# Performance work log

Hardware: AMD Instinct MI355X
Metric: run time of the kernel (lower is better)

## Reference

```python
import jax, jax.numpy as jnp
import numpy as np

B = 8
DIM = 256          # __init__ dim; input has 2*DIM channels
H = 32
W = 32
NUM_HEADS = 4
DH_QK = 64         # make_divisible(256*1.0, 8) // 4
DH_V = 64          # dim_out // num_heads
DQK = NUM_HEADS * DH_QK   # 256
DV = NUM_HEADS * DH_V     # 256
SCALE = DH_QK ** -0.5
HIDDEN = 4 * DIM          # mlp_ratio=4 applied to dim
DIM_OUT = DIM
EPS = 1e-5


def setup_inputs() -> dict:
    key = jax.random.key(0)
    ks = jax.random.split(key, 8)
    qkv_out = 2 * DQK + DV   # 768
    return {
        "x": jax.random.normal(ks[0], (B, 2 * DIM, H, W), jnp.float32),
        "qkv_f_w": jax.random.normal(ks[1], (qkv_out, DIM), jnp.float32) * DIM ** -0.5,
        "qkv_p_w": jax.random.normal(ks[2], (qkv_out, DIM), jnp.float32) * DIM ** -0.5,
        "height_rel": jax.random.normal(ks[3], (2 * H - 1, DH_QK), jnp.float32) * SCALE,
        "width_rel": jax.random.normal(ks[4], (2 * W - 1, DH_QK), jnp.float32) * SCALE,
        "ln_gamma": jnp.ones((2 * DV, H, W), jnp.float32),
        "ln_beta": jnp.zeros((2 * DV, H, W), jnp.float32),
        "fc1_w": jax.random.normal(ks[5], (HIDDEN, 2 * DV), jnp.float32) * (2 * DV) ** -0.5,
        "fc1_b": jnp.zeros((HIDDEN,), jnp.float32),
        "fc2_w": jax.random.normal(ks[6], (DIM_OUT, HIDDEN), jnp.float32) * HIDDEN ** -0.5,
        "fc2_b": jnp.zeros((DIM_OUT,), jnp.float32),
    }


def _rel_to_abs(x):
    # x: (b, L, 2L-1) -> (b, L, L) via the pad/reshape shift trick
    b, L, _ = x.shape
    x = jnp.pad(x, ((0, 0), (0, 0), (0, 1)))          # (b, L, 2L)
    xf = x.reshape(b, L * 2 * L)
    xf = jnp.pad(xf, ((0, 0), (0, L - 1)))
    return xf.reshape(b, L + 1, 2 * L - 1)[:, :L, L - 1:]


def _rel_logits_1d(q, rel_k, perm):
    # q: (b, h, w, d); rel_k: (2w-1, d) -> (b, h, w, h, w) after perm
    b, h, w, _ = q.shape
    x = jnp.einsum('bhwd,md->bhwm', q, rel_k).reshape(b * h, w, 2 * w - 1)
    x = _rel_to_abs(x).reshape(b, h, 1, w, w)
    x = jnp.broadcast_to(x, (b, h, h, w, w))
    return x.transpose(perm)


def _pos_embed(q, height_rel, width_rel):
    # q: (B*nh, HW, d) -> relative-position logits (B*nh, HW, HW)
    bh = q.shape[0]
    qs = q.reshape(bh, H, W, DH_QK)
    lw = _rel_logits_1d(qs, width_rel, (0, 1, 3, 2, 4))
    lh = _rel_logits_1d(qs.transpose(0, 2, 1, 3), height_rel, (0, 3, 1, 4, 2))
    return (lh + lw).reshape(bh, H * W, H * W)


def _get_qkv(x, w):
    # 1x1 conv as channel GEMM; x: (B, DIM, H, W)
    qkv = jnp.einsum('bchw,oc->bohw', x, w)
    q, k, v = jnp.split(qkv, [DQK, 2 * DQK], axis=1)
    q = q.reshape(B * NUM_HEADS, DH_QK, H * W).transpose(0, 2, 1)  # (Bh, HW, d)
    k = k.reshape(B * NUM_HEADS, DH_QK, H * W)                      # (Bh, d, HW)
    v = v.reshape(B * NUM_HEADS, DH_V, H * W).transpose(0, 2, 1)    # (Bh, HW, d)
    return q, k, v


def _apply_attn(q, k, v, height_rel, width_rel):
    logits = jnp.einsum('bnd,bdm->bnm', q, k) * SCALE + _pos_embed(q, height_rel, width_rel)
    attn = jax.nn.softmax(logits, axis=-1)
    out = jnp.einsum('bnm,bmd->bnd', attn, v)                       # (Bh, HW, dv)
    return out.transpose(0, 2, 1).reshape(B, DV, H, W)


def reference(x, qkv_f_w, qkv_p_w, height_rel, width_rel, ln_gamma, ln_beta,
              fc1_w, fc1_b, fc2_w, fc2_b):
    x1, x2 = x[:, :DIM], x[:, DIM:]
    qf, kf, vf = _get_qkv(x1, qkv_f_w)
    qp, kp, vp = _get_qkv(x2, qkv_p_w)
    out_f = _apply_attn(qf, kp, vp, height_rel, width_rel)
    out_p = _apply_attn(qp, kf, vf, height_rel, width_rel)
    xpf = jnp.concatenate([out_f, out_p], axis=1)                   # (B, 2*DV, H, W)
    # LayerNorm over normalized_shape = [2*DV, H, W]
    mean = xpf.mean(axis=(1, 2, 3), keepdims=True)
    var = jnp.var(xpf, axis=(1, 2, 3), keepdims=True)
    xpf = (xpf - mean) * jax.lax.rsqrt(var + EPS) * ln_gamma + ln_beta
    # conv-MLP (1x1 convs), exact GELU as torch default
    h = jnp.einsum('bchw,oc->bohw', xpf, fc1_w) + fc1_b[None, :, None, None]
    h = jax.nn.gelu(h, approximate=False)
    out = jnp.einsum('bchw,oc->bohw', h, fc2_w) + fc2_b[None, :, None, None]
    return out  # stride=1 -> pool is identity
```

## Files before the change

kernel.cpp:

```cpp
#include <hip/hip_runtime.h>

#define SCALE 0.125f

typedef short short8 __attribute__((ext_vector_type(8)));
typedef float f32x4 __attribute__((ext_vector_type(4)));
typedef unsigned short us8 __attribute__((ext_vector_type(8)));

typedef __attribute__((address_space(1))) const void gvoid;
typedef __attribute__((address_space(3))) void svoid;
__device__ __forceinline__ void gll16(const void* g, void* l) {
  __builtin_amdgcn_global_load_lds((gvoid*)g, (svoid*)l, 16, 0, 0);
}

__device__ __forceinline__ unsigned short f2bf(float x) {
  unsigned int u = __float_as_uint(x);
  u += 0x7fff + ((u >> 16) & 1);
  return (unsigned short)(u >> 16);
}
__device__ __forceinline__ float bf2f(unsigned short b) {
  return __uint_as_float(((unsigned int)b) << 16);
}
__device__ __forceinline__ float gelu_exact(float x) {
  return 0.5f * x * (1.0f + erff(x * 0.70710678118654752f));
}

__global__ __launch_bounds__(256)
void cast_w(const float* __restrict__ qf, const float* __restrict__ qp,
            const float* __restrict__ f1, const float* __restrict__ f2,
            unsigned short* __restrict__ wc)
{
  const int i4 = (blockIdx.x * 256 + threadIdx.x) * 4;
  const float* src; int off;
  if (i4 < 196608)      { src = qf; off = i4; }
  else if (i4 < 393216) { src = qp; off = i4 - 196608; }
  else if (i4 < 917504) { src = f1; off = i4 - 393216; }
  else                  { src = f2; off = i4 - 917504; }
  const float4 v = *(const float4*)(src + off);
  ushort4 o;
  o.x = f2bf(v.x); o.y = f2bf(v.y); o.z = f2bf(v.z); o.w = f2bf(v.w);
  *(ushort4*)(wc + i4) = o;
}

__global__ __launch_bounds__(256)
void trans_x(const float* __restrict__ x, unsigned short* __restrict__ xT)
{
  __shared__ unsigned short L[64 * 72];
  const int ch0 = blockIdx.x * 64, tok0 = blockIdx.y * 64, z = blockIdx.z;
  const int b = z & 7, path = z >> 3;
  const float* src = x + (size_t)b * 524288 + (size_t)(path * 256 + ch0) * 1024 + tok0;
#pragma unroll
  for (int t = 0; t < 4; ++t) {
    const int i = threadIdx.x + t * 256;
    const int row = i >> 4, c4 = (i & 15) * 4;
    const float4 v = *(const float4*)(src + (size_t)row * 1024 + c4);
    L[(c4 + 0) * 72 + row] = f2bf(v.x);
    L[(c4 + 1) * 72 + row] = f2bf(v.y);
    L[(c4 + 2) * 72 + row] = f2bf(v.z);
    L[(c4 + 3) * 72 + row] = f2bf(v.w);
  }
  __syncthreads();
  unsigned short* dst = xT + (size_t)z * 262144 + (size_t)tok0 * 256 + ch0;
#pragma unroll
  for (int t = 0; t < 2; ++t) {
    const int i = threadIdx.x + t * 256;
    const int row = i >> 3, c8 = (i & 7) * 8;
    *(us8*)(dst + (size_t)row * 256 + c8) = *(const us8*)&L[row * 72 + c8];
  }
}

__global__ __launch_bounds__(256)
void trans_gb(const float* __restrict__ gamma, const float* __restrict__ beta,
              unsigned short* __restrict__ gbT)
{
  __shared__ unsigned short L[64 * 72];
  const int ch0 = blockIdx.x * 64, tok0 = blockIdx.y * 64, which = blockIdx.z;
  const float* src = (which ? beta : gamma) + (size_t)ch0 * 1024 + tok0;
#pragma unroll
  for (int t = 0; t < 4; ++t) {
    const int i = threadIdx.x + t * 256;
    const int row = i >> 4, c4 = (i & 15) * 4;
    const float4 v = *(const float4*)(src + (size_t)row * 1024 + c4);
    L[(c4 + 0) * 72 + row] = f2bf(v.x);
    L[(c4 + 1) * 72 + row] = f2bf(v.y);
    L[(c4 + 2) * 72 + row] = f2bf(v.z);
    L[(c4 + 3) * 72 + row] = f2bf(v.w);
  }
  __syncthreads();
  unsigned short* dst = gbT + (size_t)which * 524288 + (size_t)tok0 * 512 + ch0;
#pragma unroll
  for (int t = 0; t < 2; ++t) {
    const int i = threadIdx.x + t * 256;
    const int row = i >> 3, c8 = (i & 7) * 8;
    *(us8*)(dst + (size_t)row * 512 + c8) = *(const us8*)&L[row * 72 + c8];
  }
}

template<int MODE, int LD, int KLEN>
__global__ __launch_bounds__(256, 3)
void gemm_mf(const unsigned short* __restrict__ A0, const unsigned short* __restrict__ B0,
             unsigned short* __restrict__ qkT, unsigned short* __restrict__ vb,
             unsigned short* __restrict__ hT, float* __restrict__ outF,
             const float* __restrict__ bias)
{
  __shared__ unsigned short As[2][4096];
  __shared__ unsigned short Bs[2][4096];
  const int tid = threadIdx.x;
  const int lane = tid & 63, w = tid >> 6;
  const int c = lane & 15, g = lane >> 4;
  const int wm = w >> 1, wn = w & 1;
  const int m0 = blockIdx.x * 128, n0 = blockIdx.y * 128;
  const int z = blockIdx.z;

  const unsigned short* A;
  const unsigned short* B;
  int zb = z, kc = 0;
  if (MODE == 0) {
    A = A0 + (size_t)(z >> 3) * 196608;
    B = B0 + (size_t)z * 262144;
  } else if (MODE == 1) {
    A = A0;
    B = B0 + (size_t)z * 1024 * LD;
  } else {
    zb = z >> 1; kc = z & 1;
    A = A0 + kc * KLEN;
    B = B0 + (size_t)zb * 1024 * LD + kc * KLEN;
  }

  f32x4 acc[4][4];
#pragma unroll
  for (int mi = 0; mi < 4; ++mi)
#pragma unroll
    for (int ni = 0; ni < 4; ++ni) acc[mi][ni] = (f32x4){0.f, 0.f, 0.f, 0.f};

  const int srow = tid >> 2;
  const int skc8 = (tid & 3) * 8;
  const int sbase = (tid & 192) * 8;

#pragma unroll
  for (int t = 0; t < 2; ++t) {
    gll16(A + (size_t)(m0 + srow + t * 64) * LD + skc8, &As[0][sbase + t * 2048]);
    gll16(B + (size_t)(n0 + srow + t * 64) * LD + skc8, &Bs[0][sbase + t * 2048]);
  }

  const int NK = KLEN / 32;
  for (int ks = 0; ks < NK; ++ks) {
    __syncthreads();
    if (ks + 1 < NK) {
      const int k0 = (ks + 1) * 32;
      const int nb = (ks + 1) & 1;
#pragma unroll
      for (int t = 0; t < 2; ++t) {
        gll16(A + (size_t)(m0 + srow + t * 64) * LD + k0 + skc8, &As[nb][sbase + t * 2048]);
        gll16(B + (size_t)(n0 + srow + t * 64) * LD + k0 + skc8, &Bs[nb][sbase + t * 2048]);
      }
    }
    const unsigned short* Asb = As[ks & 1];
    const unsigned short* Bsb = Bs[ks & 1];
    short8 aF[4], bF[4];
#pragma unroll
    for (int mi = 0; mi < 4; ++mi)
      aF[mi] = *(const short8*)&Asb[(64 * wm + 16 * mi + c) * 32 + g * 8];
#pragma unroll
    for (int ni = 0; ni < 4; ++ni)
      bF[ni] = *(const short8*)&Bsb[(64 * wn + 16 * ni + c) * 32 + g * 8];
#pragma unroll
    for (int mi = 0; mi < 4; ++mi)
#pragma unroll
      for (int ni = 0; ni < 4; ++ni)
        acc[mi][ni] = __builtin_amdgcn_mfma_f32_16x16x32_bf16(aF[mi], bF[ni], acc[mi][ni], 0, 0, 0);
  }

  if (MODE == 0) {
#pragma unroll
    for (int mi = 0; mi < 4; ++mi) {
      const int mb = m0 + 64 * wm + 16 * mi + 4 * g;
#pragma unroll
      for (int ni = 0; ni < 4; ++ni) {
        const int n = n0 + 64 * wn + 16 * ni + c;
        if (mb < 512) {
          ushort4 o4;
          o4.x = f2bf(acc[mi][ni][0]); o4.y = f2bf(acc[mi][ni][1]);
          o4.z = f2bf(acc[mi][ni][2]); o4.w = f2bf(acc[mi][ni][3]);
          *(ushort4*)(qkT + (size_t)z * 524288 + (size_t)n * 512 + mb) = o4;
        } else {
#pragma unroll
          for (int r = 0; r < 4; ++r)
            vb[(size_t)z * 262144 + (size_t)(mb - 512 + r) * 1024 + n] = f2bf(acc[mi][ni][r]);
        }
      }
    }
  } else if (MODE == 1) {
#pragma unroll
    for (int mi = 0; mi < 4; ++mi) {
      const int mb = m0 + 64 * wm + 16 * mi + 4 * g;
      const float4 b4 = *(const float4*)(bias + mb);
#pragma unroll
      for (int ni = 0; ni < 4; ++ni) {
        const int n = n0 + 64 * wn + 16 * ni + c;
        ushort4 o4;
        o4.x = f2bf(gelu_exact(acc[mi][ni][0] + b4.x));
        o4.y = f2bf(gelu_exact(acc[mi][ni][1] + b4.y));
        o4.z = f2bf(gelu_exact(acc[mi][ni][2] + b4.z));
        o4.w = f2bf(gelu_exact(acc[mi][ni][3] + b4.w));
        *(ushort4*)(hT + (size_t)z * 1048576 + (size_t)n * 1024 + mb) = o4;
      }
    }
  } else {
#pragma unroll
    for (int mi = 0; mi < 4; ++mi) {
      const int mb = m0 + 64 * wm + 16 * mi + 4 * g;
      float4 b4 = make_float4(0.f, 0.f, 0.f, 0.f);
      if (kc == 0) b4 = *(const float4*)(bias + mb);
#pragma unroll
      for (int ni = 0; ni < 4; ++ni) {
        const int n = n0 + 64 * wn + 16 * ni + c;
        float* op = outF + (size_t)zb * 262144 + (size_t)mb * 1024 + n;
        atomicAdd(&op[0],    acc[mi][ni][0] + b4.x);
        atomicAdd(&op[1024], acc[mi][ni][1] + b4.y);
        atomicAdd(&op[2048], acc[mi][ni][2] + b4.z);
        atomicAdd(&op[3072], acc[mi][ni][3] + b4.w);
      }
    }
  }
}

__global__ __launch_bounds__(256, 2)
void attn_k(const unsigned short* __restrict__ qkT,
            const unsigned short* __restrict__ vbuf,
            const float* __restrict__ hrel,
            const float* __restrict__ wrel,
            unsigned short* __restrict__ xpfT,
            float* __restrict__ stats)
{
  __shared__ unsigned short Kb[2][4096];
  __shared__ unsigned short Vb[2][4096];
  __shared__ unsigned short Ps[128 * 72];
  __shared__ unsigned short QHt[128 * 34];

  const int tid = threadIdx.x;
  const int lane = tid & 63, w = tid >> 6;
  const int c = lane & 15, g = lane >> 4;
  const int xb = blockIdx.x;
  const int pOut = xb >> 5, bh = xb & 31;
  const int b = bh >> 2, head = bh & 3, pKV = 1 - pOut;
  const int n0 = blockIdx.y * 128;
  const int rb = 32 * w;

  const unsigned short* Qg = qkT + (size_t)(pOut * 8 + b) * 524288 + head * 64;
  const unsigned short* Kg = qkT + (size_t)(pKV * 8 + b) * 524288 + 256 + head * 64;
  const unsigned short* Vg = vbuf + ((size_t)(pKV * 8 + b) * 256 + head * 64) * 1024;

  us8 kr[2], vr[2];
#pragma unroll
  for (int t = 0; t < 2; ++t) {
    const int i = tid + t * 256;
    const int row = i >> 3, ch = i & 7;
    kr[t] = *(const us8*)(Kg + (size_t)row * 512 + ch * 8);
    vr[t] = *(const us8*)(Vg + (size_t)row * 1024 + ch * 8);
  }

  short8 bQ[2][2];
#pragma unroll
  for (int grp = 0; grp < 2; ++grp) {
    const unsigned short* qp = Qg + (size_t)(n0 + rb + 16 * grp + c) * 512 + 8 * g;
    bQ[grp][0] = *(const short8*)(qp);
    bQ[grp][1] = *(const short8*)(qp + 32);
  }

#pragma unroll
  for (int f = 0; f < 4; ++f) {
    const int rr = 16 * f + c;
    const int rrc = rr < 63 ? rr : 62;
    const float sc = rr < 63 ? 1.f : 0.f;
    short8 w0, w1, h0, h1;
#pragma unroll
    for (int j = 0; j < 8; ++j) {
      w0[j] = f2bf(wrel[rrc * 64 + 8 * g + j] * sc);
      w1[j] = f2bf(wrel[rrc * 64 + 32 + 8 * g + j] * sc);
      h0[j] = f2bf(hrel[rrc * 64 + 8 * g + j] * sc);
      h1[j] = f2bf(hrel[rrc * 64 + 32 + 8 * g + j] * sc);
    }
#pragma unroll
    for (int grp = 0; grp < 2; ++grp) {
      f32x4 zw = {0.f, 0.f, 0.f, 0.f};
      zw = __builtin_amdgcn_mfma_f32_16x16x32_bf16(w0, bQ[grp][0], zw, 0, 0, 0);
      zw = __builtin_amdgcn_mfma_f32_16x16x32_bf16(w1, bQ[grp][1], zw, 0, 0, 0);
      f32x4 zh = {0.f, 0.f, 0.f, 0.f};
      zh = __builtin_amdgcn_mfma_f32_16x16x32_bf16(h0, bQ[grp][0], zh, 0, 0, 0);
      zh = __builtin_amdgcn_mfma_f32_16x16x32_bf16(h1, bQ[grp][1], zh, 0, 0, 0);
      const int qrow = rb + 16 * grp + c;
      ushort4 pw;
      pw.x = f2bf(zw[0]); pw.y = f2bf(zw[1]); pw.z = f2bf(zw[2]); pw.w = f2bf(zw[3]);
      *(ushort4*)&Ps[qrow * 72 + 16 * f + 4 * g] = pw;
      const int h1i = (n0 + qrow) >> 5;
#pragma unroll
      for (int r = 0; r < 4; ++r) {
        const int h2 = 16 * f + 4 * g + r - 31 + h1i;
        if (h2 >= 0 && h2 < 32) QHt[qrow * 34 + h2] = f2bf(zh[r]);
      }
    }
  }

  float qwv[2][2][4];
#pragma unroll
  for (int grp = 0; grp < 2; ++grp) {
    const int qrow = rb + 16 * grp + c;
    const int w1i = (n0 + qrow) & 31;
#pragma unroll
    for (int p = 0; p < 2; ++p)
#pragma unroll
      for (int r = 0; r < 4; ++r)
        qwv[grp][p][r] = bf2f(Ps[qrow * 72 + (16 * p + 4 * g + r - w1i + 31)]);
  }

#pragma unroll
  for (int t = 0; t < 2; ++t) {
    const int i = tid + t * 256;
    const int row = i >> 3, ch = i & 7;
    const int p = row * 64 + ((ch ^ (row & 7)) * 8);
    *(us8*)&Kb[0][p] = kr[t];
    *(us8*)&Vb[0][p] = vr[t];
  }

  float lsum[2] = {0.f, 0.f};
  f32x4 O[2][4];
#pragma unroll
  for (int grp = 0; grp < 2; ++grp)
#pragma unroll
    for (int f = 0; f < 4; ++f) O[grp][f] = (f32x4){0.f, 0.f, 0.f, 0.f};

  for (int mt = 0; mt < 16; ++mt) {
    __syncthreads();
    if (mt < 15) {
      const int m0n = (mt + 1) * 64;
#pragma unroll
      for (int t = 0; t < 2; ++t) {
        const int i = tid + t * 256;
        const int row = i >> 3, ch = i & 7;
        kr[t] = *(const us8*)(Kg + (size_t)(m0n + row) * 512 + ch * 8);
        vr[t] = *(const us8*)(Vg + (size_t)row * 1024 + m0n + ch * 8);
      }
    }
    const unsigned short* Ks = Kb[mt & 1];
    const unsigned short* Vs = Vb[mt & 1];

    short8 kA[4][2];
#pragma unroll
    for (int f = 0; f < 4; ++f) {
      const int row = 16 * f + c;
      kA[f][0] = *(const short8*)&Ks[row * 64 + ((g ^ (row & 7)) * 8)];
      kA[f][1] = *(const short8*)&Ks[row * 64 + (((4 + g) ^ (row & 7)) * 8)];
    }
#pragma unroll
    for (int grp = 0; grp < 2; ++grp) {
      const int qrow = rb + 16 * grp + c;
      const float qh0 = bf2f(QHt[qrow * 34 + 2 * mt]);
      const float qh1 = bf2f(QHt[qrow * 34 + 2 * mt + 1]);
#pragma unroll
      for (int f = 0; f < 4; ++f) {
        f32x4 z = {0.f, 0.f, 0.f, 0.f};
        z = __builtin_amdgcn_mfma_f32_16x16x32_bf16(kA[f][0], bQ[grp][0], z, 0, 0, 0);
        z = __builtin_amdgcn_mfma_f32_16x16x32_bf16(kA[f][1], bQ[grp][1], z, 0, 0, 0);
        const float qh = (f >= 2) ? qh1 : qh0;
        const float* qwp = qwv[grp][f & 1];
        const float p0 = __expf(fmaf(z[0], SCALE, qh + qwp[0]));
        const float p1 = __expf(fmaf(z[1], SCALE, qh + qwp[1]));
        const float p2 = __expf(fmaf(z[2], SCALE, qh + qwp[2]));
        const float p3 = __expf(fmaf(z[3], SCALE, qh + qwp[3]));
        lsum[grp] += (p0 + p1) + (p2 + p3);
        ushort4 pk;
        pk.x = f2bf(p0); pk.y = f2bf(p1); pk.z = f2bf(p2); pk.w = f2bf(p3);
        *(ushort4*)&Ps[qrow * 72 + 16 * f + 4 * g] = pk;
      }
    }
    short8 vB[4][2];
#pragma unroll
    for (int f = 0; f < 4; ++f) {
      const int row = 16 * f + c;
      vB[f][0] = *(const short8*)&Vs[row * 64 + ((g ^ (row & 7)) * 8)];
      vB[f][1] = *(const short8*)&Vs[row * 64 + (((4 + g) ^ (row & 7)) * 8)];
    }
#pragma unroll
    for (int grp = 0; grp < 2; ++grp) {
      const int qrow = rb + 16 * grp + c;
      const short8 aP0 = *(const short8*)&Ps[qrow * 72 + 8 * g];
      const short8 aP1 = *(const short8*)&Ps[qrow * 72 + 32 + 8 * g];
#pragma unroll
      for (int f = 0; f < 4; ++f) {
        O[grp][f] = __builtin_amdgcn_mfma_f32_16x16x32_bf16(aP0, vB[f][0], O[grp][f], 0, 0, 0);
        O[grp][f] = __builtin_amdgcn_mfma_f32_16x16x32_bf16(aP1, vB[f][1], O[grp][f], 0, 0, 0);
      }
    }
    if (mt < 15) {
#pragma unroll
      for (int t = 0; t < 2; ++t) {
        const int i = tid + t * 256;
        const int row = i >> 3, ch = i & 7;
        const int p = row * 64 + ((ch ^ (row & 7)) * 8);
        *(us8*)&Kb[(mt + 1) & 1][p] = kr[t];
        *(us8*)&Vb[(mt + 1) & 1][p] = vr[t];
      }
    }
  }

#pragma unroll
  for (int grp = 0; grp < 2; ++grp) {
    lsum[grp] += __shfl_xor(lsum[grp], 16);
    lsum[grp] += __shfl_xor(lsum[grp], 32);
  }
  float linv[2][4];
#pragma unroll
  for (int grp = 0; grp < 2; ++grp)
#pragma unroll
    for (int r = 0; r < 4; ++r)
      linv[grp][r] = 1.0f / __shfl(lsum[grp], 4 * g + r);

  float ssum = 0.f, ssq = 0.f;
#pragma unroll
  for (int grp = 0; grp < 2; ++grp)
#pragma unroll
    for (int f = 0; f < 4; ++f)
#pragma unroll
      for (int r = 0; r < 4; ++r) {
        const float v = O[grp][f][r] * linv[grp][r];
        ssum += v;
        ssq = fmaf(v, v, ssq);
        Ps[(rb + 16 * grp + 4 * g + r) * 72 + 16 * f + c] = f2bf(v);
      }
#pragma unroll
  for (int off = 1; off < 64; off <<= 1) {
    ssum += __shfl_xor(ssum, off);
    ssq  += __shfl_xor(ssq, off);
  }
  if (lane == 0) {
    atomicAdd(&stats[b * 2 + 0], ssum);
    atomicAdd(&stats[b * 2 + 1], ssq);
  }

  __syncthreads();
  unsigned short* dst = xpfT + ((size_t)b * 1024 + n0) * 512 + pOut * 256 + head * 64;
#pragma unroll
  for (int t = 0; t < 4; ++t) {
    const int i = tid + t * 256;
    const int row = i >> 3, ch = i & 7;
    *(us8*)(dst + (size_t)row * 512 + ch * 8) = *(const us8*)&Ps[row * 72 + ch * 8];
  }
}

__global__ __launch_bounds__(256)
void ln_k(const unsigned short* __restrict__ xpfT, const unsigned short* __restrict__ gbT,
          const float* __restrict__ stats, unsigned short* __restrict__ xln)
{
  const int i = blockIdx.x * 256 + threadIdx.x;
  const int b = i >> 16, off = i & 65535;
  const float invN = 1.0f / 524288.0f;
  const float mean = stats[b * 2] * invN;
  const float var = stats[b * 2 + 1] * invN - mean * mean;
  const float rstd = rsqrtf(var + 1e-5f);
  const us8 xv = *(const us8*)(xpfT + (size_t)i * 8);
  const us8 gv = *(const us8*)(gbT + (size_t)off * 8);
  const us8 bv = *(const us8*)(gbT + 524288 + (size_t)off * 8);
  us8 ov;
#pragma unroll
  for (int j = 0; j < 8; ++j)
    ov[j] = f2bf((bf2f(xv[j]) - mean) * rstd * bf2f(gv[j]) + bf2f(bv[j]));
  *(us8*)(xln + (size_t)i * 8) = ov;
}

extern "C" void kernel_launch(void* const* d_in, const int* in_sizes, int n_in,
                              void* d_out, int out_size, void* d_ws, size_t ws_size,
                              hipStream_t stream)
{
  const float* x     = (const float*)d_in[0];
  const float* qkvfw = (const float*)d_in[1];
  const float* qkvpw = (const float*)d_in[2];
  const float* hrel  = (const float*)d_in[3];
  const float* wrel  = (const float*)d_in[4];
  const float* gamma = (const float*)d_in[5];
  const float* beta  = (const float*)d_in[6];
  const float* fc1w  = (const float*)d_in[7];
  const float* fc1b  = (const float*)d_in[8];
  const float* fc2w  = (const float*)d_in[9];
  const float* fc2b  = (const float*)d_in[10];
  float* out = (float*)d_out;

  float* stats = (float*)d_ws;
  unsigned short* wc   = (unsigned short*)(stats + 64);
  unsigned short* xT   = wc + 1179648;
  unsigned short* gbT  = xT + 4194304;
  unsigned short* qkT  = gbT + 1048576;
  unsigned short* vbuf = qkT + 8388608;
  unsigned short* xpfT = vbuf + 4194304;
  unsigned short* hT   = xpfT + 4194304;

  hipMemsetAsync(stats, 0, 64 * sizeof(float), stream);
  hipMemsetAsync(out, 0, (size_t)out_size * sizeof(float), stream);

  cast_w<<<1152, 256, 0, stream>>>(qkvfw, qkvpw, fc1w, fc2w, wc);
  trans_x<<<dim3(4, 16, 16), 256, 0, stream>>>(x, xT);
  trans_gb<<<dim3(8, 16, 2), 256, 0, stream>>>(gamma, beta, gbT);

  gemm_mf<0, 256, 256><<<dim3(6, 8, 16), 256, 0, stream>>>(
      wc, xT, qkT, vbuf, nullptr, nullptr, nullptr);

  attn_k<<<dim3(64, 8), 256, 0, stream>>>(qkT, vbuf, hrel, wrel, xpfT, stats);

  ln_k<<<2048, 256, 0, stream>>>(xpfT, gbT, stats, xT);

  gemm_mf<1, 512, 512><<<dim3(8, 8, 8), 256, 0, stream>>>(
      wc + 393216, xT, nullptr, nullptr, hT, nullptr, fc1b);

  gemm_mf<3, 1024, 512><<<dim3(2, 8, 16), 256, 0, stream>>>(
      wc + 917504, hT, nullptr, nullptr, nullptr, out, fc2b);
}
```

Baseline: 249.5 us.

## Halve attention query tile, merge prep kernels, deepen fc2 split-K

The attention kernel now processes 64 query rows per block instead of 128, with one 16-row group per wave. It packs its LDS into a single swizzled buffer and raises the launch bound to 4 blocks per CU, doubling grid parallelism and occupancy. The three preprocessing kernels (weight cast, x transpose, gamma/beta transpose) are merged into one launch to cut launch overhead. The fc2 GEMM split-K goes from 2 to 4 chunks, giving more blocks at the cost of more atomic adds on the output and K/V tiles being reloaded by twice as many attention blocks.

```diff
diff --git a/kernel.cpp b/kernel.cpp
--- a/kernel.cpp
+++ b/kernel.cpp
@@ -25,32 +25,48 @@
 }
 
 __global__ __launch_bounds__(256)
-void cast_w(const float* __restrict__ qf, const float* __restrict__ qp,
+void prep_k(const float* __restrict__ qf, const float* __restrict__ qp,
             const float* __restrict__ f1, const float* __restrict__ f2,
-            unsigned short* __restrict__ wc)
-{
-  const int i4 = (blockIdx.x * 256 + threadIdx.x) * 4;
-  const float* src; int off;
-  if (i4 < 196608)      { src = qf; off = i4; }
-  else if (i4 < 393216) { src = qp; off = i4 - 196608; }
-  else if (i4 < 917504) { src = f1; off = i4 - 393216; }
-  else                  { src = f2; off = i4 - 917504; }
-  const float4 v = *(const float4*)(src + off);
-  ushort4 o;
-  o.x = f2bf(v.x); o.y = f2bf(v.y); o.z = f2bf(v.z); o.w = f2bf(v.w);
-  *(ushort4*)(wc + i4) = o;
-}
-
-__global__ __launch_bounds__(256)
-void trans_x(const float* __restrict__ x, unsigned short* __restrict__ xT)
+            const float* __restrict__ x, const float* __restrict__ gamma,
+            const float* __restrict__ beta, unsigned short* __restrict__ wc,
+            unsigned short* __restrict__ xT, unsigned short* __restrict__ gbT)
 {
   __shared__ unsigned short L[64 * 72];
-  const int ch0 = blockIdx.x * 64, tok0 = blockIdx.y * 64, z = blockIdx.z;
-  const int b = z & 7, path = z >> 3;
-  const float* src = x + (size_t)b * 524288 + (size_t)(path * 256 + ch0) * 1024 + tok0;
+  const int bx = blockIdx.x;
+  const int tid = threadIdx.x;
+  if (bx < 1152) {
+    const int i4 = (bx * 256 + tid) * 4;
+    const float* src; int off;
+    if (i4 < 196608)      { src = qf; off = i4; }
+    else if (i4 < 393216) { src = qp; off = i4 - 196608; }
+    else if (i4 < 917504) { src = f1; off = i4 - 393216; }
+    else                  { src = f2; off = i4 - 917504; }
+    const float4 v = *(const float4*)(src + off);
+    ushort4 o;
+    o.x = f2bf(v.x); o.y = f2bf(v.y); o.z = f2bf(v.z); o.w = f2bf(v.w);
+    *(ushort4*)(wc + i4) = o;
+    return;
+  }
+  const float* src;
+  unsigned short* dst;
+  int dstride;
+  if (bx < 2176) {
+    const int t = bx - 1152;
+    const int ch0 = (t & 3) * 64, tok0 = ((t >> 2) & 15) * 64, z = t >> 6;
+    const int b = z & 7, path = z >> 3;
+    src = x + (size_t)b * 524288 + (size_t)(path * 256 + ch0) * 1024 + tok0;
+    dst = xT + (size_t)z * 262144 + (size_t)tok0 * 256 + ch0;
+    dstride = 256;
+  } else {
+    const int u = bx - 2176;
+    const int ch0 = (u & 7) * 64, tok0 = ((u >> 3) & 15) * 64, which = u >> 7;
+    src = (which ? beta : gamma) + (size_t)ch0 * 1024 + tok0;
+    dst = gbT + (size_t)which * 524288 + (size_t)tok0 * 512 + ch0;
+    dstride = 512;
+  }
 #pragma unroll
   for (int t = 0; t < 4; ++t) {
-    const int i = threadIdx.x + t * 256;
+    const int i = tid + t * 256;
     const int row = i >> 4, c4 = (i & 15) * 4;
     const float4 v = *(const float4*)(src + (size_t)row * 1024 + c4);
     L[(c4 + 0) * 72 + row] = f2bf(v.x);
@@ -59,39 +75,11 @@
     L[(c4 + 3) * 72 + row] = f2bf(v.w);
   }
   __syncthreads();
-  unsigned short* dst = xT + (size_t)z * 262144 + (size_t)tok0 * 256 + ch0;
 #pragma unroll
   for (int t = 0; t < 2; ++t) {
-    const int i = threadIdx.x + t * 256;
+    const int i = tid + t * 256;
     const int row = i >> 3, c8 = (i & 7) * 8;
-    *(us8*)(dst + (size_t)row * 256 + c8) = *(const us8*)&L[row * 72 + c8];
-  }
-}
-
-__global__ __launch_bounds__(256)
-void trans_gb(const float* __restrict__ gamma, const float* __restrict__ beta,
-              unsigned short* __restrict__ gbT)
-{
-  __shared__ unsigned short L[64 * 72];
-  const int ch0 = blockIdx.x * 64, tok0 = blockIdx.y * 64, which = blockIdx.z;
-  const float* src = (which ? beta : gamma) + (size_t)ch0 * 1024 + tok0;
-#pragma unroll
-  for (int t = 0; t < 4; ++t) {
-    const int i = threadIdx.x + t * 256;
-    const int row = i >> 4, c4 = (i & 15) * 4;
-    const float4 v = *(const float4*)(src + (size_t)row * 1024 + c4);
-    L[(c4 + 0) * 72 + row] = f2bf(v.x);
-    L[(c4 + 1) * 72 + row] = f2bf(v.y);
-    L[(c4 + 2) * 72 + row] = f2bf(v.z);
-    L[(c4 + 3) * 72 + row] = f2bf(v.w);
-  }
-  __syncthreads();
-  unsigned short* dst = gbT + (size_t)which * 524288 + (size_t)tok0 * 512 + ch0;
-#pragma unroll
-  for (int t = 0; t < 2; ++t) {
-    const int i = threadIdx.x + t * 256;
-    const int row = i >> 3, c8 = (i & 7) * 8;
-    *(us8*)(dst + (size_t)row * 512 + c8) = *(const us8*)&L[row * 72 + c8];
+    *(us8*)(dst + (size_t)row * dstride + c8) = *(const us8*)&L[row * 72 + c8];
   }
 }
 
@@ -121,7 +109,7 @@
     A = A0;
     B = B0 + (size_t)z * 1024 * LD;
   } else {
-    zb = z >> 1; kc = z & 1;
+    zb = z >> 2; kc = z & 3;
     A = A0 + kc * KLEN;
     B = B0 + (size_t)zb * 1024 * LD + kc * KLEN;
   }
@@ -224,7 +212,7 @@
   }
 }
 
-__global__ __launch_bounds__(256, 2)
+__global__ __launch_bounds__(256, 4)
 void attn_k(const unsigned short* __restrict__ qkT,
             const unsigned short* __restrict__ vbuf,
             const float* __restrict__ hrel,
@@ -232,10 +220,9 @@
             unsigned short* __restrict__ xpfT,
             float* __restrict__ stats)
 {
-  __shared__ unsigned short Kb[2][4096];
-  __shared__ unsigned short Vb[2][4096];
-  __shared__ unsigned short Ps[128 * 72];
-  __shared__ unsigned short QHt[128 * 34];
+  __shared__ unsigned short lds[20480];
+  unsigned short* Ps  = lds + 16384;
+  unsigned short* QHt = lds + 8192;
 
   const int tid = threadIdx.x;
   const int lane = tid & 63, w = tid >> 6;
@@ -243,13 +230,17 @@
   const int xb = blockIdx.x;
   const int pOut = xb >> 5, bh = xb & 31;
   const int b = bh >> 2, head = bh & 3, pKV = 1 - pOut;
-  const int n0 = blockIdx.y * 128;
-  const int rb = 32 * w;
+  const int n0 = blockIdx.y * 64;
+  const int rb = 16 * w;
+  const int qrow = rb + c;
+  const int qs7 = qrow & 7;
 
   const unsigned short* Qg = qkT + (size_t)(pOut * 8 + b) * 524288 + head * 64;
   const unsigned short* Kg = qkT + (size_t)(pKV * 8 + b) * 524288 + 256 + head * 64;
   const unsigned short* Vg = vbuf + ((size_t)(pKV * 8 + b) * 256 + head * 64) * 1024;
 
+  const int srow = (tid + 0) >> 3;
+  (void)srow;
   us8 kr[2], vr[2];
 #pragma unroll
   for (int t = 0; t < 2; ++t) {
@@ -259,13 +250,9 @@
     vr[t] = *(const us8*)(Vg + (size_t)row * 1024 + ch * 8);
   }
 
-  short8 bQ[2][2];
-#pragma unroll
-  for (int grp = 0; grp < 2; ++grp) {
-    const unsigned short* qp = Qg + (size_t)(n0 + rb + 16 * grp + c) * 512 + 8 * g;
-    bQ[grp][0] = *(const short8*)(qp);
-    bQ[grp][1] = *(const short8*)(qp + 32);
-  }
+  const unsigned short* qp = Qg + (size_t)(n0 + qrow) * 512 + 8 * g;
+  const short8 bQ0 = *(const short8*)(qp);
+  const short8 bQ1 = *(const short8*)(qp + 32);
 
 #pragma unroll
   for (int f = 0; f < 4; ++f) {
@@ -280,55 +267,52 @@
       h0[j] = f2bf(hrel[rrc * 64 + 8 * g + j] * sc);
       h1[j] = f2bf(hrel[rrc * 64 + 32 + 8 * g + j] * sc);
     }
-#pragma unroll
-    for (int grp = 0; grp < 2; ++grp) {
-      f32x4 zw = {0.f, 0.f, 0.f, 0.f};
-      zw = __builtin_amdgcn_mfma_f32_16x16x32_bf16(w0, bQ[grp][0], zw, 0, 0, 0);
-      zw = __builtin_amdgcn_mfma_f32_16x16x32_bf16(w1, bQ[grp][1], zw, 0, 0, 0);
-      f32x4 zh = {0.f, 0.f, 0.f, 0.f};
-      zh = __builtin_amdgcn_mfma_f32_16x16x32_bf16(h0, bQ[grp][0], zh, 0, 0, 0);
-      zh = __builtin_amdgcn_mfma_f32_16x16x32_bf16(h1, bQ[grp][1], zh, 0, 0, 0);
-      const int qrow = rb + 16 * grp + c;
-      ushort4 pw;
-      pw.x = f2bf(zw[0]); pw.y = f2bf(zw[1]); pw.z = f2bf(zw[2]); pw.w = f2bf(zw[3]);
-      *(ushort4*)&Ps[qrow * 72 + 16 * f + 4 * g] = pw;
-      const int h1i = (n0 + qrow) >> 5;
-#pragma unroll
-      for (int r = 0; r < 4; ++r) {
-        const int h2 = 16 * f + 4 * g + r - 31 + h1i;
-        if (h2 >= 0 && h2 < 32) QHt[qrow * 34 + h2] = f2bf(zh[r]);
-      }
-    }
-  }
-
-  float qwv[2][2][4];
-#pragma unroll
-  for (int grp = 0; grp < 2; ++grp) {
-    const int qrow = rb + 16 * grp + c;
-    const int w1i = (n0 + qrow) & 31;
-#pragma unroll
-    for (int p = 0; p < 2; ++p)
-#pragma unroll
-      for (int r = 0; r < 4; ++r)
-        qwv[grp][p][r] = bf2f(Ps[qrow * 72 + (16 * p + 4 * g + r - w1i + 31)]);
-  }
+    f32x4 zw = {0.f, 0.f, 0.f, 0.f};
+    zw = __builtin_amdgcn_mfma_f32_16x16x32_bf16(w0, bQ0, zw, 0, 0, 0);
+    zw = __builtin_amdgcn_mfma_f32_16x16x32_bf16(w1, bQ1, zw, 0, 0, 0);
+    f32x4 zh = {0.f, 0.f, 0.f, 0.f};
+    zh = __builtin_amdgcn_mfma_f32_16x16x32_bf16(h0, bQ0, zh, 0, 0, 0);
+    zh = __builtin_amdgcn_mfma_f32_16x16x32_bf16(h1, bQ1, zh, 0, 0, 0);
+    ushort4 pw;
+    pw.x = f2bf(zw[0]); pw.y = f2bf(zw[1]); pw.z = f2bf(zw[2]); pw.w = f2bf(zw[3]);
+    *(ushort4*)&Ps[qrow * 64 + (((2 * f + (g >> 1)) ^ qs7) * 8) + (g & 1) * 4] = pw;
+    const int h1i = (n0 + qrow) >> 5;
+#pragma unroll
+    for (int r = 0; r < 4; ++r) {
+      const int h2 = 16 * f + 4 * g + r - 31 + h1i;
+      if (h2 >= 0 && h2 < 32) QHt[qrow * 40 + h2] = f2bf(zh[r]);
+    }
+  }
+
+  const int w1i = (n0 + qrow) & 31;
+  float qwv[2][4];
+#pragma unroll
+  for (int p = 0; p < 2; ++p)
+#pragma unroll
+    for (int r = 0; r < 4; ++r) {
+      const int col = 16 * p + 4 * g + r - w1i + 31;
+      qwv[p][r] = bf2f(Ps[qrow * 64 + (((col >> 3) ^ qs7) * 8) + (col & 7)]);
+    }
+
+  us8 qh4[4];
+#pragma unroll
+  for (int t = 0; t < 4; ++t) qh4[t] = *(const us8*)&QHt[qrow * 40 + 8 * t];
 
 #pragma unroll
   for (int t = 0; t < 2; ++t) {
     const int i = tid + t * 256;
     const int row = i >> 3, ch = i & 7;
     const int p = row * 64 + ((ch ^ (row & 7)) * 8);
-    *(us8*)&Kb[0][p] = kr[t];
-    *(us8*)&Vb[0][p] = vr[t];
-  }
-
-  float lsum[2] = {0.f, 0.f};
-  f32x4 O[2][4];
-#pragma unroll
-  for (int grp = 0; grp < 2; ++grp)
-#pragma unroll
-    for (int f = 0; f < 4; ++f) O[grp][f] = (f32x4){0.f, 0.f, 0.f, 0.f};
-
+    *(us8*)&lds[p] = kr[t];
+    *(us8*)&lds[4096 + p] = vr[t];
+  }
+
+  float lsum = 0.f;
+  f32x4 O[4];
+#pragma unroll
+  for (int f = 0; f < 4; ++f) O[f] = (f32x4){0.f, 0.f, 0.f, 0.f};
+
+#pragma unroll
   for (int mt = 0; mt < 16; ++mt) {
     __syncthreads();
     if (mt < 15) {
@@ -341,92 +325,76 @@
         vr[t] = *(const us8*)(Vg + (size_t)row * 1024 + m0n + ch * 8);
       }
     }
-    const unsigned short* Ks = Kb[mt & 1];
-    const unsigned short* Vs = Vb[mt & 1];
-
-    short8 kA[4][2];
+    const unsigned short* Ks = lds + (mt & 1) * 8192;
+    const unsigned short* Vs = lds + 4096 + (mt & 1) * 8192;
+
+    const float qh0 = bf2f(qh4[mt >> 2][(mt & 3) * 2]);
+    const float qh1 = bf2f(qh4[mt >> 2][(mt & 3) * 2 + 1]);
+
+    f32x4 Sf[4];
 #pragma unroll
     for (int f = 0; f < 4; ++f) {
       const int row = 16 * f + c;
-      kA[f][0] = *(const short8*)&Ks[row * 64 + ((g ^ (row & 7)) * 8)];
-      kA[f][1] = *(const short8*)&Ks[row * 64 + (((4 + g) ^ (row & 7)) * 8)];
-    }
-#pragma unroll
-    for (int grp = 0; grp < 2; ++grp) {
-      const int qrow = rb + 16 * grp + c;
-      const float qh0 = bf2f(QHt[qrow * 34 + 2 * mt]);
-      const float qh1 = bf2f(QHt[qrow * 34 + 2 * mt + 1]);
-#pragma unroll
-      for (int f = 0; f < 4; ++f) {
-        f32x4 z = {0.f, 0.f, 0.f, 0.f};
-        z = __builtin_amdgcn_mfma_f32_16x16x32_bf16(kA[f][0], bQ[grp][0], z, 0, 0, 0);
-        z = __builtin_amdgcn_mfma_f32_16x16x32_bf16(kA[f][1], bQ[grp][1], z, 0, 0, 0);
-        const float qh = (f >= 2) ? qh1 : qh0;
-        const float* qwp = qwv[grp][f & 1];
-        const float p0 = __expf(fmaf(z[0], SCALE, qh + qwp[0]));
-        const float p1 = __expf(fmaf(z[1], SCALE, qh + qwp[1]));
-        const float p2 = __expf(fmaf(z[2], SCALE, qh + qwp[2]));
-        const float p3 = __expf(fmaf(z[3], SCALE, qh + qwp[3]));
-        lsum[grp] += (p0 + p1) + (p2 + p3);
-        ushort4 pk;
-        pk.x = f2bf(p0); pk.y = f2bf(p1); pk.z = f2bf(p2); pk.w = f2bf(p3);
-        *(ushort4*)&Ps[qrow * 72 + 16 * f + 4 * g] = pk;
-      }
-    }
-    short8 vB[4][2];
+      const short8 kA0 = *(const short8*)&Ks[row * 64 + ((g ^ (row & 7)) * 8)];
+      const short8 kA1 = *(const short8*)&Ks[row * 64 + (((4 + g) ^ (row & 7)) * 8)];
+      f32x4 z = {0.f, 0.f, 0.f, 0.f};
+      z = __builtin_amdgcn_mfma_f32_16x16x32_bf16(kA0, bQ0, z, 0, 0, 0);
+      z = __builtin_amdgcn_mfma_f32_16x16x32_bf16(kA1, bQ1, z, 0, 0, 0);
+      Sf[f] = z;
+    }
+#pragma unroll
+    for (int f = 0; f < 4; ++f) {
+      const float qh = (f >= 2) ? qh1 : qh0;
+      const float* qwp = qwv[f & 1];
+      const float p0 = __expf(fmaf(Sf[f][0], SCALE, qh + qwp[0]));
+      const float p1 = __expf(fmaf(Sf[f][1], SCALE, qh + qwp[1]));
+      const float p2 = __expf(fmaf(Sf[f][2], SCALE, qh + qwp[2]));
+      const float p3 = __expf(fmaf(Sf[f][3], SCALE, qh + qwp[3]));
+      lsum += (p0 + p1) + (p2 + p3);
+      ushort4 pk;
+      pk.x = f2bf(p0); pk.y = f2bf(p1); pk.z = f2bf(p2); pk.w = f2bf(p3);
+      *(ushort4*)&Ps[qrow * 64 + (((2 * f + (g >> 1)) ^ qs7) * 8) + (g & 1) * 4] = pk;
+    }
+    const short8 aP0 = *(const short8*)&Ps[qrow * 64 + ((g ^ qs7) * 8)];
+    const short8 aP1 = *(const short8*)&Ps[qrow * 64 + (((4 + g) ^ qs7) * 8)];
 #pragma unroll
     for (int f = 0; f < 4; ++f) {
       const int row = 16 * f + c;
-      vB[f][0] = *(const short8*)&Vs[row * 64 + ((g ^ (row & 7)) * 8)];
-      vB[f][1] = *(const short8*)&Vs[row * 64 + (((4 + g) ^ (row & 7)) * 8)];
-    }
-#pragma unroll
-    for (int grp = 0; grp < 2; ++grp) {
-      const int qrow = rb + 16 * grp + c;
-      const short8 aP0 = *(const short8*)&Ps[qrow * 72 + 8 * g];
-      const short8 aP1 = *(const short8*)&Ps[qrow * 72 + 32 + 8 * g];
-#pragma unroll
-      for (int f = 0; f < 4; ++f) {
-        O[grp][f] = __builtin_amdgcn_mfma_f32_16x16x32_bf16(aP0, vB[f][0], O[grp][f], 0, 0, 0);
-        O[grp][f] = __builtin_amdgcn_mfma_f32_16x16x32_bf16(aP1, vB[f][1], O[grp][f], 0, 0, 0);
-      }
+      const short8 vB0 = *(const short8*)&Vs[row * 64 + ((g ^ (row & 7)) * 8)];
+      const short8 vB1 = *(const short8*)&Vs[row * 64 + (((4 + g) ^ (row & 7)) * 8)];
+      O[f] = __builtin_amdgcn_mfma_f32_16x16x32_bf16(aP0, vB0, O[f], 0, 0, 0);
+      O[f] = __builtin_amdgcn_mfma_f32_16x16x32_bf16(aP1, vB1, O[f], 0, 0, 0);
     }
     if (mt < 15) {
+      const int nb = (mt + 1) & 1;
 #pragma unroll
       for (int t = 0; t < 2; ++t) {
         const int i = tid + t * 256;
         const int row = i >> 3, ch = i & 7;
         const int p = row * 64 + ((ch ^ (row & 7)) * 8);
-        *(us8*)&Kb[(mt + 1) & 1][p] = kr[t];
-        *(us8*)&Vb[(mt + 1) & 1][p] = vr[t];
-      }
-    }
-  }
-
-#pragma unroll
-  for (int grp = 0; grp < 2; ++grp) {
-    lsum[grp] += __shfl_xor(lsum[grp], 16);
-    lsum[grp] += __shfl_xor(lsum[grp], 32);
-  }
-  float linv[2][4];
-#pragma unroll
-  for (int grp = 0; grp < 2; ++grp)
-#pragma unroll
-    for (int r = 0; r < 4; ++r)
-      linv[grp][r] = 1.0f / __shfl(lsum[grp], 4 * g + r);
+        *(us8*)&lds[nb * 8192 + p] = kr[t];
+        *(us8*)&lds[4096 + nb * 8192 + p] = vr[t];
+      }
+    }
+  }
+
+  lsum += __shfl_xor(lsum, 16);
+  lsum += __shfl_xor(lsum, 32);
+  float linv[4];
+#pragma unroll
+  for (int r = 0; r < 4; ++r) linv[r] = 1.0f / __shfl(lsum, 4 * g + r);
 
   float ssum = 0.f, ssq = 0.f;
 #pragma unroll
-  for (int grp = 0; grp < 2; ++grp)
-#pragma unroll
-    for (int f = 0; f < 4; ++f)
-#pragma unroll
-      for (int r = 0; r < 4; ++r) {
-        const float v = O[grp][f][r] * linv[grp][r];
-        ssum += v;
-        ssq = fmaf(v, v, ssq);
-        Ps[(rb + 16 * grp + 4 * g + r) * 72 + 16 * f + c] = f2bf(v);
-      }
+  for (int f = 0; f < 4; ++f)
+#pragma unroll
+    for (int r = 0; r < 4; ++r) {
+      const float v = O[f][r] * linv[r];
+      ssum += v;
+      ssq = fmaf(v, v, ssq);
+      const int orow = rb + 4 * g + r;
+      Ps[orow * 64 + (((2 * f + (c >> 3)) ^ (orow & 7)) * 8) + (c & 7)] = f2bf(v);
+    }
 #pragma unroll
   for (int off = 1; off < 64; off <<= 1) {
     ssum += __shfl_xor(ssum, off);
@@ -440,10 +408,10 @@
   __syncthreads();
   unsigned short* dst = xpfT + ((size_t)b * 1024 + n0) * 512 + pOut * 256 + head * 64;
 #pragma unroll
-  for (int t = 0; t < 4; ++t) {
+  for (int t = 0; t < 2; ++t) {
     const int i = tid + t * 256;
     const int row = i >> 3, ch = i & 7;
-    *(us8*)(dst + (size_t)row * 512 + ch * 8) = *(const us8*)&Ps[row * 72 + ch * 8];
+    *(us8*)(dst + (size_t)row * 512 + ch * 8) = *(const us8*)&Ps[row * 64 + ((ch ^ (row & 7)) * 8)];
   }
 }
 
@@ -496,20 +464,19 @@
   hipMemsetAsync(stats, 0, 64 * sizeof(float), stream);
   hipMemsetAsync(out, 0, (size_t)out_size * sizeof(float), stream);
 
-  cast_w<<<1152, 256, 0, stream>>>(qkvfw, qkvpw, fc1w, fc2w, wc);
-  trans_x<<<dim3(4, 16, 16), 256, 0, stream>>>(x, xT);
-  trans_gb<<<dim3(8, 16, 2), 256, 0, stream>>>(gamma, beta, gbT);
+  prep_k<<<2432, 256, 0, stream>>>(qkvfw, qkvpw, fc1w, fc2w, x, gamma, beta,
+                                   wc, xT, gbT);
 
   gemm_mf<0, 256, 256><<<dim3(6, 8, 16), 256, 0, stream>>>(
       wc, xT, qkT, vbuf, nullptr, nullptr, nullptr);
 
-  attn_k<<<dim3(64, 8), 256, 0, stream>>>(qkT, vbuf, hrel, wrel, xpfT, stats);
+  attn_k<<<dim3(64, 16), 256, 0, stream>>>(qkT, vbuf, hrel, wrel, xpfT, stats);
 
   ln_k<<<2048, 256, 0, stream>>>(xpfT, gbT, stats, xT);
 
   gemm_mf<1, 512, 512><<<dim3(8, 8, 8), 256, 0, stream>>>(
       wc + 393216, xT, nullptr, nullptr, hT, nullptr, fc1b);
 
-  gemm_mf<3, 1024, 512><<<dim3(2, 8, 16), 256, 0, stream>>>(
+  gemm_mf<3, 1024, 256><<<dim3(2, 8, 32), 256, 0, stream>>>(
       wc + 917504, hT, nullptr, nullptr, nullptr, out, fc2b);
 }
```

Measured after the change: 315.7 us. 1.27x slower.
